# Optimization experiments

Measured on AMD Instinct MI355X. Metric: run time of the kernel, lower is better.

The kernel has to match this reference:

```python
import jax, jax.numpy as jnp
import numpy as np

L_SEG = 20   # number of CFT segments (hard-coded in original forward)
M_CHEB = 8   # Chebyshev quadrature order per segment


def _cft_magnitude(x, modes):
    """|CFT(x)| at integer frequencies [0, modes).

    Faithful to vectorized_batched_cft_decomposed with L=20, M=8, but only
    evaluated at the first `modes` frequencies (identical values; the original
    computes all rfft freqs then slices). Segment loop is folded into a single
    einsum by absorbing the per-segment phase shift into the quadrature weights.
    x: (B, C, N) real. Returns (B, C, modes) float.
    """
    n = x.shape[-1]
    t = jnp.linspace(0.0, 1.0, n)
    freqs = jnp.arange(modes, dtype=x.dtype)  # rfftfreq(n, d=1/n)[:modes]
    seg_len = 1.0 / L_SEG
    starts = jnp.linspace(0.0, 1.0, L_SEG + 1)[:-1]  # (L,)
    k = jnp.arange(M_CHEB, dtype=x.dtype)
    cheb = -jnp.cos((2.0 * k + 1.0) * jnp.pi / (2.0 * M_CHEB))  # (M,) nodes in [-1,1]
    T = jnp.cos(k[:, None] * jnp.arccos(cheb)[None, :])  # (K=M, M) Chebyshev T_k at nodes
    angle = cheb[:, None] * (freqs[None, :] * (2.0 * jnp.pi * seg_len / 2.0))  # (M, F)
    Wr = jnp.einsum('km,mf->kf', T, jnp.cos(angle)) * (seg_len / 2.0)  # (M, F)
    Wi = jnp.einsum('km,mf->kf', T, -jnp.sin(angle)) * (seg_len / 2.0)
    # piecewise-linear interpolation of x at the Chebyshev nodes of every segment
    t_seg = starts[:, None] + seg_len / 2.0 * (cheb + 1.0)[None, :]  # (L, M)
    right = jnp.clip(jnp.searchsorted(t, t_seg), 0, n - 1)
    left = jnp.clip(right - 1, 0, None)
    t_l, t_r = t[left], t[right]
    denom = jnp.where(t_r - t_l == 0.0, 1.0, t_r - t_l)
    w_r = (t_seg - t_l) / denom
    w_l = 1.0 - w_r
    seg = w_l * x[:, :, left] + w_r * x[:, :, right]  # (B, C, L, M)
    # per-segment phase shift exp(-i*2*pi*f*a) folded into combined weights
    phi = 2.0 * jnp.pi * starts[:, None] * freqs[None, :]  # (L, F)
    cs, sn = jnp.cos(phi), jnp.sin(phi)
    Ar = Wr[None] * cs[:, None, :] + Wi[None] * sn[:, None, :]   # (L, M, F)
    Ai = -Wr[None] * sn[:, None, :] + Wi[None] * cs[:, None, :]
    real = jnp.einsum('bclm,lmf->bcf', seg, Ar)
    imag = jnp.einsum('bclm,lmf->bcf', seg, Ai)
    return jnp.sqrt(real * real + imag * imag)


def setup_inputs() -> dict:
    key = jax.random.key(0)
    ks = jax.random.split(key, 4)
    B, Cin, Cout, N, modes = 32, 64, 64, 8192, 32
    scale = 1.0 / (Cin * Cout)
    return {
        'x': jax.random.normal(ks[0], (B, Cin, N), dtype=jnp.float32),
        'w1_real': scale * jax.random.uniform(ks[1], (Cin, Cout, modes), dtype=jnp.float32),
        'w1_imag': scale * jax.random.uniform(ks[2], (Cin, Cout, modes), dtype=jnp.float32),
        'gate_w': jax.random.normal(ks[3], (Cout, Cin), dtype=jnp.float32) / np.sqrt(Cin),
        'ln_gamma': jnp.ones((modes,), dtype=jnp.float32),
        'ln_beta': jnp.zeros((modes,), dtype=jnp.float32),
    }


def reference(x, w1_real, w1_imag, gate_w, ln_gamma, ln_beta):
    n = x.shape[-1]
    n_rfft = n // 2 + 1
    modes = w1_real.shape[-1]
    x_fft = jnp.fft.rfft(x)  # (B, C, n_rfft) complex64
    # CFT magnitude is detached in the original (x_cft.detach())
    mag = jax.lax.stop_gradient(_cft_magnitude(x, modes))  # (B, C, modes)
    # LayerNorm over the modes axis (eps = 1e-5, torch default)
    mu = jnp.mean(mag, axis=-1, keepdims=True)
    var = jnp.mean((mag - mu) ** 2, axis=-1, keepdims=True)
    g_norm = (mag - mu) / jnp.sqrt(var + 1e-5) * ln_gamma + ln_beta
    # 1x1 conv (no bias) over channels, then sigmoid gate
    gate = jax.nn.sigmoid(jnp.einsum('oi,bif->bof', gate_w, g_norm))  # (B, Cout, modes)
    gated = x_fft[:, :, :modes] * gate  # requires Cin == Cout
    w1 = w1_real + 1j * w1_imag  # (Cin, Cout, modes) complex
    out_modes = jnp.einsum('bix,iox->box', gated, w1)
    pad = jnp.zeros(out_modes.shape[:2] + (n_rfft - modes,), dtype=out_modes.dtype)
    out_ft = jnp.concatenate([out_modes, pad], axis=-1)
    return jnp.fft.irfft(out_ft, n=n)
```

## Files before the change

kernel.cpp:

```cpp
#include <hip/hip_runtime.h>
#include <hip/hip_bf16.h>
#include <math.h>

#define NN    8192
#define NH    4096
#define NROWS 2048
#define FF    32
#define LM    160

static constexpr int TRIG   = 0;
static constexpr int W1RT   = 524288;
static constexpr int W1IT   = 655360;
static constexpr int GWT    = 786432;
static constexpr int AR_    = 790528;
static constexpr int AI_    = 795648;
static constexpr int WL_    = 800768;
static constexpr int WR_    = 800928;
static constexpr int IL_    = 801088;
static constexpr int IR_    = 801248;
static constexpr int XR_    = 801408;
static constexpr int XI_    = 866944;
static constexpr int GN_    = 932480;
static constexpr int ARAI   = 998016;
static constexpr int TRIGT_ = 1129088;

#define PI_D 3.14159265358979323846

__device__ __forceinline__ void load_lds16(const float* g, float* l) {
  __builtin_amdgcn_global_load_lds(
      (const __attribute__((address_space(1))) void*)g,
      (__attribute__((address_space(3))) void*)l, 16, 0, 0);
}

__global__ __launch_bounds__(256) void k_trig(float* __restrict__ ws) {
  int idx = blockIdx.x * 256 + threadIdx.x;
  int k4 = idx >> 8, f = (idx >> 2) & 63, e = idx & 3;
  int n = 4 * k4 + e;
  int fr = f & 31;
  int p = (fr * n) & (NN - 1);
  float ang = (float)p * (float)(2.0 * PI_D / (double)NN);
  float s, c;
  sincosf(ang, &s, &c);
  float v = (f < 32) ? c : s;
  ws[TRIG + idx] = v;
  ws[TRIGT_ + f * NH + n] = v;
}

__global__ __launch_bounds__(256) void k_cft_tables(float* __restrict__ ws) {
  int tid = blockIdx.x * 256 + threadIdx.x;
  if (tid >= LM * FF) return;
  int j = tid >> 5, f = tid & 31;
  int l = j >> 3, m = j & 7;
  const double cheb[8] = {
    -0.98078528040323044913, -0.83146961230254523708,
    -0.55557023301960222474, -0.19509032201612826785,
     0.19509032201612826785,  0.55557023301960222474,
     0.83146961230254523708,  0.98078528040323044913 };

  double Wr = 0.0, Wi = 0.0;
  #pragma unroll
  for (int mm = 0; mm < 8; ++mm) {
    double c = cheb[mm];
    double T;
    if (m == 0) T = 1.0;
    else {
      double a = 1.0, b = c;
      for (int q = 1; q < m; ++q) { double t = 2.0 * c * b - a; a = b; b = t; }
      T = b;
    }
    double ang = c * (double)f * (PI_D * 0.05);
    Wr += T * cos(ang);
    Wi += T * (-sin(ang));
  }
  Wr *= 0.025; Wi *= 0.025;
  double phi = 2.0 * PI_D * ((double)l * 0.05) * (double)f;
  double cs = cos(phi), sn = sin(phi);
  ws[AR_ + j * FF + f] = (float)(Wr * cs + Wi * sn);
  ws[AI_ + j * FF + f] = (float)(-Wr * sn + Wi * cs);

  if (f == 0) {
    double v = (double)l * 0.05 + 0.025 * (cheb[m] + 1.0);
    int r = (int)(v * 8191.0);
    while ((double)r / 8191.0 < v) ++r;
    while (r > 0 && (double)(r - 1) / 8191.0 >= v) --r;
    if (r > 8191) r = 8191;
    int le = r - 1; if (le < 0) le = 0;
    double tl = (double)le / 8191.0, tr = (double)r / 8191.0;
    double den = (tr - tl == 0.0) ? 1.0 : (tr - tl);
    double wr = (v - tl) / den;
    ws[WL_ + j] = (float)(1.0 - wr);
    ws[WR_ + j] = (float)wr;
    ((int*)ws)[IL_ + j] = le;
    ((int*)ws)[IR_ + j] = r;
  }
}

__global__ __launch_bounds__(256) void k_transpose(const float* __restrict__ w1r,
                                                   const float* __restrict__ w1i,
                                                   const float* __restrict__ gw,
                                                   float* __restrict__ ws) {
  int idx = blockIdx.x * 256 + threadIdx.x;
  if (idx >= 32 * 64 * 64) return;
  int o = idx & 63, i = (idx >> 6) & 63, f = idx >> 12;
  ws[W1RT + (f * 64 + i) * 64 + o] = w1r[(i * 64 + o) * FF + f];
  ws[W1IT + (f * 64 + i) * 64 + o] = w1i[(i * 64 + o) * FF + f];
  if (idx < 4096) {
    ws[GWT + idx] = gw[(idx & 63) * 64 + (idx >> 6)];
  }
}

__global__ __launch_bounds__(256) void k_fwd_gemm(const float* __restrict__ x,
                                                  const float* __restrict__ ws,
                                                  float* __restrict__ part) {
  __shared__ __align__(16) float uw[4096 + 16 + 4096];
  __shared__ __align__(16) float ts[16 * 256];
  const int rt = blockIdx.x >> 6, jc = blockIdx.x & 63;
  const int t = threadIdx.x;
  const int w = t >> 6, lane = t & 63;
  const int half = lane >> 5, fl = lane & 31;
  const int rblock = rt * 64;
  const int jb = jc * 64;

  const float* __restrict__ tsrc = ws + TRIG + (size_t)jc * 4096;
  #pragma unroll
  for (int p = 0; p < 4; ++p) {
    int q = 256 * p + t;
    load_lds16(tsrc + q * 4, &ts[q * 4]);
  }

  #pragma unroll
  for (int p = 0; p < 4; ++p) {
    int idx = 256 * p + t;
    int row = idx >> 4, c4 = idx & 15;
    const float* __restrict__ xp = x + (size_t)(rblock + row) * NN + jb + c4 * 4;
    float4 a = *(const float4*)xp;
    float4 b = *(const float4*)(xp + NH);
    float4 u = make_float4(a.x + b.x, a.y + b.y, a.z + b.z, a.w + b.w);
    float4 v = make_float4(a.x - b.x, a.y - b.y, a.z - b.z, a.w - b.w);
    *(float4*)(&uw[row * 64 + c4 * 4]) = u;
    *(float4*)(&uw[4112 + row * 64 + c4 * 4]) = v;
  }

  float accC[8], accS[8];
  #pragma unroll
  for (int r = 0; r < 8; ++r) { accC[r] = 0.f; accS[r] = 0.f; }

  __syncthreads();

  const float* __restrict__ xb = &uw[(fl & 1) * 4112 + (w * 16 + half * 8) * 64];
  const float* __restrict__ tb = &ts[fl * 4];

  #pragma unroll
  for (int it = 0; it < 16; ++it) {
    float4 tc = *(const float4*)(tb + it * 256);
    float4 tn = *(const float4*)(tb + it * 256 + 128);
    #pragma unroll
    for (int j = 0; j < 8; ++j) {
      float4 xv = *(const float4*)(xb + j * 64 + it * 4);
      accC[j] = fmaf(xv.w, tc.w, fmaf(xv.z, tc.z,
                fmaf(xv.y, tc.y, fmaf(xv.x, tc.x, accC[j]))));
      accS[j] = fmaf(xv.w, tn.w, fmaf(xv.z, tn.z,
                fmaf(xv.y, tn.y, fmaf(xv.x, tn.x, accS[j]))));
    }
  }

  float* __restrict__ pp = part + ((size_t)jc * NROWS + rblock + w * 16 + half * 8) * 64;
  #pragma unroll
  for (int j = 0; j < 8; ++j) {
    pp[j * 64 + fl]      = accC[j];
    pp[j * 64 + 32 + fl] = accS[j];
  }
}

__global__ __launch_bounds__(256) void k_fred(const float* __restrict__ part,
                                              float* __restrict__ ws) {
  int idx = blockIdx.x * 256 + threadIdx.x;
  int row = idx >> 4, fq = idx & 15;
  const float4* __restrict__ p4 = (const float4*)part;
  float4 s = make_float4(0.f, 0.f, 0.f, 0.f);
  #pragma unroll 16
  for (int kc = 0; kc < 64; ++kc) {
    float4 v = p4[((size_t)kc * NROWS + row) * 16 + fq];
    s.x += v.x; s.y += v.y; s.z += v.z; s.w += v.w;
  }
  if (fq < 8) {
    *(float4*)(ws + XR_ + row * FF + fq * 4) = s;
  } else {
    float4 n = make_float4(-s.x, -s.y, -s.z, -s.w);
    *(float4*)(ws + XI_ + row * FF + (fq - 8) * 4) = n;
  }
}

__global__ __launch_bounds__(256) void k_cft(const float* __restrict__ x,
                                             const float* __restrict__ gamma,
                                             const float* __restrict__ beta,
                                             float* __restrict__ ws) {
  const int sub = threadIdx.x >> 6, li = threadIdx.x & 63;
  const int row = blockIdx.x * 4 + sub;
  const float* __restrict__ xr = x + (size_t)row * NN;
  __shared__ float seg[4][LM];
  #pragma unroll
  for (int g = 0; g < 3; ++g) {
    int j = li + 64 * g;
    if (j < LM) {
      int il = ((const int*)ws)[IL_ + j];
      int ir = ((const int*)ws)[IR_ + j];
      seg[sub][j] = ws[WL_ + j] * xr[il] + ws[WR_ + j] * xr[ir];
    }
  }
  __syncthreads();
  if (li < FF) {
    float re = 0.f, im = 0.f;
    #pragma unroll 8
    for (int j = 0; j < LM; ++j) {
      float sv = seg[sub][j];
      re = fmaf(sv, ws[AR_ + j * FF + li], re);
      im = fmaf(sv, ws[AI_ + j * FF + li], im);
    }
    float mag = sqrtf(re * re + im * im);
    float mu = mag;
    mu += __shfl_xor(mu, 1);  mu += __shfl_xor(mu, 2);  mu += __shfl_xor(mu, 4);
    mu += __shfl_xor(mu, 8);  mu += __shfl_xor(mu, 16);
    mu *= (1.0f / 32.0f);
    float d = mag - mu;
    float vv = d * d;
    vv += __shfl_xor(vv, 1);  vv += __shfl_xor(vv, 2);  vv += __shfl_xor(vv, 4);
    vv += __shfl_xor(vv, 8);  vv += __shfl_xor(vv, 16);
    vv *= (1.0f / 32.0f);
    float g = d / sqrtf(vv + 1e-5f) * gamma[li] + beta[li];
    ws[GN_ + row * FF + li] = g;
  }
}

__global__ __launch_bounds__(64) void k_gate(float* __restrict__ ws) {
  int bidx = blockIdx.x;
  int b = bidx >> 5, f = bidx & 31;
  int o = threadIdx.x;
  __shared__ float gn[64], gr[64], gi[64];
  int rowb = b * 64;
  gn[o] = ws[GN_ + (rowb + o) * FF + f];
  float xre = ws[XR_ + (rowb + o) * FF + f];
  float xim = ws[XI_ + (rowb + o) * FF + f];
  __syncthreads();
  float acc = 0.f;
  #pragma unroll 16
  for (int i = 0; i < 64; ++i)
    acc = fmaf(ws[GWT + i * 64 + o], gn[i], acc);
  float gate = 1.0f / (1.0f + expf(-acc));
  gr[o] = xre * gate;
  gi[o] = xim * gate;
  __syncthreads();
  float Yr = 0.f, Yi = 0.f;
  const float* __restrict__ w1rt = ws + W1RT + f * 4096;
  const float* __restrict__ w1it = ws + W1IT + f * 4096;
  #pragma unroll 8
  for (int i = 0; i < 64; ++i) {
    float a = gr[i], bb2 = gi[i];
    float wr = w1rt[i * 64 + o], wi = w1it[i * 64 + o];
    Yr = fmaf(a, wr, Yr); Yr = fmaf(-bb2, wi, Yr);
    Yi = fmaf(a, wi, Yi); Yi = fmaf(bb2, wr, Yi);
  }
  float* A = ws + ARAI + (size_t)(rowb + o) * 64;
  if (f == 0) {
    A[0]  = Yr * (1.0f / (float)NN);
    A[32] = 0.0f;
  } else {
    A[f]      = Yr * (2.0f / (float)NN);
    A[32 + f] = -Yi * (2.0f / (float)NN);
  }
}

__global__ __launch_bounds__(256) void k_inv(const float* __restrict__ ws,
                                             float* __restrict__ out) {
  __shared__ __align__(16) float As[32 * 64];
  const int blk = blockIdx.x;
  const int bb = blk >> 4, cc = blk & 15;
  const int t = threadIdx.x;
  const int w = t >> 6, lane = t & 63;
  const int rowbase = bb * 32;
  const float* __restrict__ trigt = ws + TRIGT_;
  const int colb = cc * 256 + lane * 4;

  float4 tg0 = *(const float4*)(trigt + (size_t)0 * NH + colb);
  float4 tg1 = *(const float4*)(trigt + (size_t)1 * NH + colb);
  float4 tg2 = *(const float4*)(trigt + (size_t)2 * NH + colb);
  float4 tg3 = *(const float4*)(trigt + (size_t)3 * NH + colb);

  #pragma unroll
  for (int p = 0; p < 2; ++p) {
    int idx = t + 256 * p;
    int r = idx >> 4, q = idx & 15;
    *(float4*)(&As[r * 64 + q * 4]) =
        *(const float4*)(ws + ARAI + (size_t)(rowbase + r) * 64 + q * 4);
  }

  float4 accE[8], accO[8];
  #pragma unroll
  for (int r = 0; r < 8; ++r) {
    accE[r] = make_float4(0.f, 0.f, 0.f, 0.f);
    accO[r] = make_float4(0.f, 0.f, 0.f, 0.f);
  }

  __syncthreads();

#define INV_STEP(F0)                                                            \
  {                                                                             \
    _Pragma("unroll")                                                           \
    for (int r = 0; r < 8; ++r) {                                               \
      float4 av = *(const float4*)(&As[(w * 8 + r) * 64 + (F0)]);               \
      accE[r].x = fmaf(av.x, tg0.x, accE[r].x); accE[r].y = fmaf(av.x, tg0.y, accE[r].y); \
      accE[r].z = fmaf(av.x, tg0.z, accE[r].z); accE[r].w = fmaf(av.x, tg0.w, accE[r].w); \
      accO[r].x = fmaf(av.y, tg1.x, accO[r].x); accO[r].y = fmaf(av.y, tg1.y, accO[r].y); \
      accO[r].z = fmaf(av.y, tg1.z, accO[r].z); accO[r].w = fmaf(av.y, tg1.w, accO[r].w); \
      accE[r].x = fmaf(av.z, tg2.x, accE[r].x); accE[r].y = fmaf(av.z, tg2.y, accE[r].y); \
      accE[r].z = fmaf(av.z, tg2.z, accE[r].z); accE[r].w = fmaf(av.z, tg2.w, accE[r].w); \
      accO[r].x = fmaf(av.w, tg3.x, accO[r].x); accO[r].y = fmaf(av.w, tg3.y, accO[r].y); \
      accO[r].z = fmaf(av.w, tg3.z, accO[r].z); accO[r].w = fmaf(av.w, tg3.w, accO[r].w); \
    }                                                                           \
  }

  for (int fo = 0; fo < 15; ++fo) {
    int f0 = fo * 4;
    float4 n0 = *(const float4*)(trigt + (size_t)(f0 + 4) * NH + colb);
    float4 n1 = *(const float4*)(trigt + (size_t)(f0 + 5) * NH + colb);
    float4 n2 = *(const float4*)(trigt + (size_t)(f0 + 6) * NH + colb);
    float4 n3 = *(const float4*)(trigt + (size_t)(f0 + 7) * NH + colb);
    INV_STEP(f0);
    tg0 = n0; tg1 = n1; tg2 = n2; tg3 = n3;
  }
  INV_STEP(60);
#undef INV_STEP

  #pragma unroll
  for (int r = 0; r < 8; ++r) {
    int row = rowbase + w * 8 + r;
    float4 E = accE[r], O = accO[r];
    float4 s0 = make_float4(E.x + O.x, E.y + O.y, E.z + O.z, E.w + O.w);
    float4 s1 = make_float4(E.x - O.x, E.y - O.y, E.z - O.z, E.w - O.w);
    *(float4*)(out + (size_t)row * NN + colb)      = s0;
    *(float4*)(out + (size_t)row * NN + colb + NH) = s1;
  }
}

extern "C" void kernel_launch(void* const* d_in, const int* in_sizes, int n_in,
                              void* d_out, int out_size, void* d_ws, size_t ws_size,
                              hipStream_t stream) {
  const float* x     = (const float*)d_in[0];
  const float* w1r   = (const float*)d_in[1];
  const float* w1i   = (const float*)d_in[2];
  const float* gw    = (const float*)d_in[3];
  const float* gamma = (const float*)d_in[4];
  const float* beta  = (const float*)d_in[5];
  float* out = (float*)d_out;
  float* ws = (float*)d_ws;
  float* part = (float*)d_out;

  hipLaunchKernelGGL(k_trig,       dim3(1024), dim3(256), 0, stream, ws);
  hipLaunchKernelGGL(k_cft_tables, dim3(20),   dim3(256), 0, stream, ws);
  hipLaunchKernelGGL(k_transpose,  dim3(512),  dim3(256), 0, stream, w1r, w1i, gw, ws);
  hipLaunchKernelGGL(k_fwd_gemm,   dim3(2048), dim3(256), 0, stream, x, ws, part);
  hipLaunchKernelGGL(k_fred,       dim3(128),  dim3(256), 0, stream, part, ws);
  hipLaunchKernelGGL(k_cft,        dim3(512),  dim3(256), 0, stream, x, gamma, beta, ws);
  hipLaunchKernelGGL(k_gate,       dim3(1024), dim3(64),  0, stream, ws);
  hipLaunchKernelGGL(k_inv,        dim3(1024), dim3(256), 0, stream, ws, out);
}
```

Baseline: 179.9 us.

## Merge setup kernels and fold CFT into forward GEMM launch, read trig from global

Merges the three table/transpose kernels into one k_setup launch, and folds the CFT/LayerNorm kernel into the forward DFT GEMM kernel as extra blocks. In the GEMM path, the twiddle table is no longer staged in LDS; each lane now reads it straight from global memory with a one-step register prefetch. This cuts launch count from 8 to 5, lowers LDS use per block, and lets the CFT work overlap the GEMM. The cost is more global or L2 traffic for the twiddles and possible latency stalls in the inner loop.

Result: no change. 178.3 us (-0.9%).

```diff
diff --git a/kernel.cpp b/kernel.cpp
--- a/kernel.cpp
+++ b/kernel.cpp
@@ -26,149 +26,198 @@
 
 #define PI_D 3.14159265358979323846
 
-__device__ __forceinline__ void load_lds16(const float* g, float* l) {
-  __builtin_amdgcn_global_load_lds(
-      (const __attribute__((address_space(1))) void*)g,
-      (__attribute__((address_space(3))) void*)l, 16, 0, 0);
-}
-
-__global__ __launch_bounds__(256) void k_trig(float* __restrict__ ws) {
-  int idx = blockIdx.x * 256 + threadIdx.x;
-  int k4 = idx >> 8, f = (idx >> 2) & 63, e = idx & 3;
-  int n = 4 * k4 + e;
-  int fr = f & 31;
-  int p = (fr * n) & (NN - 1);
-  float ang = (float)p * (float)(2.0 * PI_D / (double)NN);
-  float s, c;
-  sincosf(ang, &s, &c);
-  float v = (f < 32) ? c : s;
-  ws[TRIG + idx] = v;
-  ws[TRIGT_ + f * NH + n] = v;
-}
-
-__global__ __launch_bounds__(256) void k_cft_tables(float* __restrict__ ws) {
-  int tid = blockIdx.x * 256 + threadIdx.x;
-  if (tid >= LM * FF) return;
-  int j = tid >> 5, f = tid & 31;
-  int l = j >> 3, m = j & 7;
-  const double cheb[8] = {
-    -0.98078528040323044913, -0.83146961230254523708,
-    -0.55557023301960222474, -0.19509032201612826785,
-     0.19509032201612826785,  0.55557023301960222474,
-     0.83146961230254523708,  0.98078528040323044913 };
-
-  double Wr = 0.0, Wi = 0.0;
-  #pragma unroll
-  for (int mm = 0; mm < 8; ++mm) {
-    double c = cheb[mm];
-    double T;
-    if (m == 0) T = 1.0;
-    else {
-      double a = 1.0, b = c;
-      for (int q = 1; q < m; ++q) { double t = 2.0 * c * b - a; a = b; b = t; }
-      T = b;
-    }
-    double ang = c * (double)f * (PI_D * 0.05);
-    Wr += T * cos(ang);
-    Wi += T * (-sin(ang));
-  }
-  Wr *= 0.025; Wi *= 0.025;
-  double phi = 2.0 * PI_D * ((double)l * 0.05) * (double)f;
-  double cs = cos(phi), sn = sin(phi);
-  ws[AR_ + j * FF + f] = (float)(Wr * cs + Wi * sn);
-  ws[AI_ + j * FF + f] = (float)(-Wr * sn + Wi * cs);
-
-  if (f == 0) {
-    double v = (double)l * 0.05 + 0.025 * (cheb[m] + 1.0);
-    int r = (int)(v * 8191.0);
-    while ((double)r / 8191.0 < v) ++r;
-    while (r > 0 && (double)(r - 1) / 8191.0 >= v) --r;
-    if (r > 8191) r = 8191;
-    int le = r - 1; if (le < 0) le = 0;
-    double tl = (double)le / 8191.0, tr = (double)r / 8191.0;
-    double den = (tr - tl == 0.0) ? 1.0 : (tr - tl);
-    double wr = (v - tl) / den;
-    ws[WL_ + j] = (float)(1.0 - wr);
-    ws[WR_ + j] = (float)wr;
-    ((int*)ws)[IL_ + j] = le;
-    ((int*)ws)[IR_ + j] = r;
-  }
-}
-
-__global__ __launch_bounds__(256) void k_transpose(const float* __restrict__ w1r,
-                                                   const float* __restrict__ w1i,
-                                                   const float* __restrict__ gw,
-                                                   float* __restrict__ ws) {
-  int idx = blockIdx.x * 256 + threadIdx.x;
-  if (idx >= 32 * 64 * 64) return;
-  int o = idx & 63, i = (idx >> 6) & 63, f = idx >> 12;
-  ws[W1RT + (f * 64 + i) * 64 + o] = w1r[(i * 64 + o) * FF + f];
-  ws[W1IT + (f * 64 + i) * 64 + o] = w1i[(i * 64 + o) * FF + f];
-  if (idx < 4096) {
-    ws[GWT + idx] = gw[(idx & 63) * 64 + (idx >> 6)];
-  }
-}
-
-__global__ __launch_bounds__(256) void k_fwd_gemm(const float* __restrict__ x,
-                                                  const float* __restrict__ ws,
-                                                  float* __restrict__ part) {
-  __shared__ __align__(16) float uw[4096 + 16 + 4096];
-  __shared__ __align__(16) float ts[16 * 256];
-  const int rt = blockIdx.x >> 6, jc = blockIdx.x & 63;
+__global__ __launch_bounds__(256) void k_setup(const float* __restrict__ w1r,
+                                               const float* __restrict__ w1i,
+                                               const float* __restrict__ gw,
+                                               float* __restrict__ ws) {
+  const int bid = blockIdx.x, tid = threadIdx.x;
+
+  if (bid < 1024) {
+    int idx = bid * 256 + tid;
+    int k4 = idx >> 8, f = (idx >> 2) & 63, e = idx & 3;
+    int n = 4 * k4 + e;
+    int fr = f & 31;
+    int p = (fr * n) & (NN - 1);
+    float ang = (float)p * (float)(2.0 * PI_D / (double)NN);
+    float s, c;
+    sincosf(ang, &s, &c);
+    float v = (f < 32) ? c : s;
+    ws[TRIG + idx] = v;
+    ws[TRIGT_ + f * NH + n] = v;
+    return;
+  }
+
+  if (bid < 1044) {
+    int t2 = (bid - 1024) * 256 + tid;
+    if (t2 >= LM * FF) return;
+    int j = t2 >> 5, f = t2 & 31;
+    int l = j >> 3, m = j & 7;
+    const double cheb[8] = {
+      -0.98078528040323044913, -0.83146961230254523708,
+      -0.55557023301960222474, -0.19509032201612826785,
+       0.19509032201612826785,  0.55557023301960222474,
+       0.83146961230254523708,  0.98078528040323044913 };
+
+    double Wr = 0.0, Wi = 0.0;
+    #pragma unroll
+    for (int mm = 0; mm < 8; ++mm) {
+      double c = cheb[mm];
+      double T;
+      if (m == 0) T = 1.0;
+      else {
+        double a = 1.0, b = c;
+        for (int q = 1; q < m; ++q) { double t = 2.0 * c * b - a; a = b; b = t; }
+        T = b;
+      }
+      double ang = c * (double)f * (PI_D * 0.05);
+      Wr += T * cos(ang);
+      Wi += T * (-sin(ang));
+    }
+    Wr *= 0.025; Wi *= 0.025;
+    double phi = 2.0 * PI_D * ((double)l * 0.05) * (double)f;
+    double cs = cos(phi), sn = sin(phi);
+    ws[AR_ + j * FF + f] = (float)(Wr * cs + Wi * sn);
+    ws[AI_ + j * FF + f] = (float)(-Wr * sn + Wi * cs);
+
+    if (f == 0) {
+      double v = (double)l * 0.05 + 0.025 * (cheb[m] + 1.0);
+      int r = (int)(v * 8191.0);
+      while ((double)r / 8191.0 < v) ++r;
+      while (r > 0 && (double)(r - 1) / 8191.0 >= v) --r;
+      if (r > 8191) r = 8191;
+      int le = r - 1; if (le < 0) le = 0;
+      double tl = (double)le / 8191.0, tr = (double)r / 8191.0;
+      double den = (tr - tl == 0.0) ? 1.0 : (tr - tl);
+      double wr = (v - tl) / den;
+      ws[WL_ + j] = (float)(1.0 - wr);
+      ws[WR_ + j] = (float)wr;
+      ((int*)ws)[IL_ + j] = le;
+      ((int*)ws)[IR_ + j] = r;
+    }
+    return;
+  }
+
+  {
+    int idx = (bid - 1044) * 256 + tid;
+    if (idx >= 32 * 64 * 64) return;
+    int o = idx & 63, i = (idx >> 6) & 63, f = idx >> 12;
+    ws[W1RT + (f * 64 + i) * 64 + o] = w1r[(i * 64 + o) * FF + f];
+    ws[W1IT + (f * 64 + i) * 64 + o] = w1i[(i * 64 + o) * FF + f];
+    if (idx < 4096) {
+      ws[GWT + idx] = gw[(idx & 63) * 64 + (idx >> 6)];
+    }
+  }
+}
+
+__global__ __launch_bounds__(256) void k_fwd(const float* __restrict__ x,
+                                             float* __restrict__ ws,
+                                             float* __restrict__ part,
+                                             const float* __restrict__ gamma,
+                                             const float* __restrict__ beta) {
+  __shared__ __align__(16) float smem[4096 + 16 + 4096];
+  const int bid = blockIdx.x;
   const int t = threadIdx.x;
-  const int w = t >> 6, lane = t & 63;
-  const int half = lane >> 5, fl = lane & 31;
-  const int rblock = rt * 64;
-  const int jb = jc * 64;
-
-  const float* __restrict__ tsrc = ws + TRIG + (size_t)jc * 4096;
-  #pragma unroll
-  for (int p = 0; p < 4; ++p) {
-    int q = 256 * p + t;
-    load_lds16(tsrc + q * 4, &ts[q * 4]);
-  }
-
-  #pragma unroll
-  for (int p = 0; p < 4; ++p) {
-    int idx = 256 * p + t;
-    int row = idx >> 4, c4 = idx & 15;
-    const float* __restrict__ xp = x + (size_t)(rblock + row) * NN + jb + c4 * 4;
-    float4 a = *(const float4*)xp;
-    float4 b = *(const float4*)(xp + NH);
-    float4 u = make_float4(a.x + b.x, a.y + b.y, a.z + b.z, a.w + b.w);
-    float4 v = make_float4(a.x - b.x, a.y - b.y, a.z - b.z, a.w - b.w);
-    *(float4*)(&uw[row * 64 + c4 * 4]) = u;
-    *(float4*)(&uw[4112 + row * 64 + c4 * 4]) = v;
-  }
-
-  float accC[8], accS[8];
-  #pragma unroll
-  for (int r = 0; r < 8; ++r) { accC[r] = 0.f; accS[r] = 0.f; }
-
-  __syncthreads();
-
-  const float* __restrict__ xb = &uw[(fl & 1) * 4112 + (w * 16 + half * 8) * 64];
-  const float* __restrict__ tb = &ts[fl * 4];
-
-  #pragma unroll
-  for (int it = 0; it < 16; ++it) {
-    float4 tc = *(const float4*)(tb + it * 256);
-    float4 tn = *(const float4*)(tb + it * 256 + 128);
+
+  if (bid < 2048) {
+    const int rt = bid >> 6, jc = bid & 63;
+    const int w = t >> 6, lane = t & 63;
+    const int half = lane >> 5, fl = lane & 31;
+    const int rblock = rt * 64;
+    const int jb = jc * 64;
+
+    #pragma unroll
+    for (int p = 0; p < 4; ++p) {
+      int idx = 256 * p + t;
+      int row = idx >> 4, c4 = idx & 15;
+      const float* __restrict__ xp = x + (size_t)(rblock + row) * NN + jb + c4 * 4;
+      float4 a = *(const float4*)xp;
+      float4 b = *(const float4*)(xp + NH);
+      float4 u = make_float4(a.x + b.x, a.y + b.y, a.z + b.z, a.w + b.w);
+      float4 v = make_float4(a.x - b.x, a.y - b.y, a.z - b.z, a.w - b.w);
+      *(float4*)(&smem[row * 64 + c4 * 4]) = u;
+      *(float4*)(&smem[4112 + row * 64 + c4 * 4]) = v;
+    }
+
+    float accC[8], accS[8];
+    #pragma unroll
+    for (int r = 0; r < 8; ++r) { accC[r] = 0.f; accS[r] = 0.f; }
+
+    __syncthreads();
+
+    const float* __restrict__ xb = &smem[(fl & 1) * 4112 + (w * 16 + half * 8) * 64];
+    const float4* __restrict__ tg4 = (const float4*)(ws + TRIG);
+    const size_t gb = (size_t)(jc * 16) * 64;
+
+#define FWD_STEP(IT, TC, TS)                                                    \
+    {                                                                           \
+      _Pragma("unroll")                                                         \
+      for (int j = 0; j < 8; ++j) {                                             \
+        float4 xv = *(const float4*)(xb + j * 64 + (IT) * 4);                   \
+        accC[j] = fmaf(xv.w, (TC).w, fmaf(xv.z, (TC).z,                         \
+                  fmaf(xv.y, (TC).y, fmaf(xv.x, (TC).x, accC[j]))));            \
+        accS[j] = fmaf(xv.w, (TS).w, fmaf(xv.z, (TS).z,                         \
+                  fmaf(xv.y, (TS).y, fmaf(xv.x, (TS).x, accS[j]))));            \
+      }                                                                         \
+    }
+
+    float4 tc = tg4[gb + fl];
+    float4 tn = tg4[gb + 32 + fl];
+    #pragma unroll 5
+    for (int it = 0; it < 15; ++it) {
+      float4 tc2 = tg4[gb + (size_t)(it + 1) * 64 + fl];
+      float4 tn2 = tg4[gb + (size_t)(it + 1) * 64 + 32 + fl];
+      FWD_STEP(it, tc, tn);
+      tc = tc2; tn = tn2;
+    }
+    FWD_STEP(15, tc, tn);
+#undef FWD_STEP
+
+    float* __restrict__ pp = part + ((size_t)jc * NROWS + rblock + w * 16 + half * 8) * 64;
     #pragma unroll
     for (int j = 0; j < 8; ++j) {
-      float4 xv = *(const float4*)(xb + j * 64 + it * 4);
-      accC[j] = fmaf(xv.w, tc.w, fmaf(xv.z, tc.z,
-                fmaf(xv.y, tc.y, fmaf(xv.x, tc.x, accC[j]))));
-      accS[j] = fmaf(xv.w, tn.w, fmaf(xv.z, tn.z,
-                fmaf(xv.y, tn.y, fmaf(xv.x, tn.x, accS[j]))));
-    }
-  }
-
-  float* __restrict__ pp = part + ((size_t)jc * NROWS + rblock + w * 16 + half * 8) * 64;
-  #pragma unroll
-  for (int j = 0; j < 8; ++j) {
-    pp[j * 64 + fl]      = accC[j];
-    pp[j * 64 + 32 + fl] = accS[j];
+      pp[j * 64 + fl]      = accC[j];
+      pp[j * 64 + 32 + fl] = accS[j];
+    }
+    return;
+  }
+
+  {
+    const int cb = bid - 2048;
+    const int sub = t >> 6, li = t & 63;
+    const int row = cb * 4 + sub;
+    const float* __restrict__ xr = x + (size_t)row * NN;
+    float (*seg)[LM] = (float (*)[LM])smem;
+    #pragma unroll
+    for (int g = 0; g < 3; ++g) {
+      int j = li + 64 * g;
+      if (j < LM) {
+        int il = ((const int*)ws)[IL_ + j];
+        int ir = ((const int*)ws)[IR_ + j];
+        seg[sub][j] = ws[WL_ + j] * xr[il] + ws[WR_ + j] * xr[ir];
+      }
+    }
+    __syncthreads();
+    if (li < FF) {
+      float re = 0.f, im = 0.f;
+      #pragma unroll 8
+      for (int j = 0; j < LM; ++j) {
+        float sv = seg[sub][j];
+        re = fmaf(sv, ws[AR_ + j * FF + li], re);
+        im = fmaf(sv, ws[AI_ + j * FF + li], im);
+      }
+      float mag = sqrtf(re * re + im * im);
+      float mu = mag;
+      mu += __shfl_xor(mu, 1);  mu += __shfl_xor(mu, 2);  mu += __shfl_xor(mu, 4);
+      mu += __shfl_xor(mu, 8);  mu += __shfl_xor(mu, 16);
+      mu *= (1.0f / 32.0f);
+      float d = mag - mu;
+      float vv = d * d;
+      vv += __shfl_xor(vv, 1);  vv += __shfl_xor(vv, 2);  vv += __shfl_xor(vv, 4);
+      vv += __shfl_xor(vv, 8);  vv += __shfl_xor(vv, 16);
+      vv *= (1.0f / 32.0f);
+      float g = d / sqrtf(vv + 1e-5f) * gamma[li] + beta[li];
+      ws[GN_ + row * FF + li] = g;
+    }
   }
 }
 
@@ -188,47 +237,6 @@
   } else {
     float4 n = make_float4(-s.x, -s.y, -s.z, -s.w);
     *(float4*)(ws + XI_ + row * FF + (fq - 8) * 4) = n;
-  }
-}
-
-__global__ __launch_bounds__(256) void k_cft(const float* __restrict__ x,
-                                             const float* __restrict__ gamma,
-                                             const float* __restrict__ beta,
-                                             float* __restrict__ ws) {
-  const int sub = threadIdx.x >> 6, li = threadIdx.x & 63;
-  const int row = blockIdx.x * 4 + sub;
-  const float* __restrict__ xr = x + (size_t)row * NN;
-  __shared__ float seg[4][LM];
-  #pragma unroll
-  for (int g = 0; g < 3; ++g) {
-    int j = li + 64 * g;
-    if (j < LM) {
-      int il = ((const int*)ws)[IL_ + j];
-      int ir = ((const int*)ws)[IR_ + j];
-      seg[sub][j] = ws[WL_ + j] * xr[il] + ws[WR_ + j] * xr[ir];
-    }
-  }
-  __syncthreads();
-  if (li < FF) {
-    float re = 0.f, im = 0.f;
-    #pragma unroll 8
-    for (int j = 0; j < LM; ++j) {
-      float sv = seg[sub][j];
-      re = fmaf(sv, ws[AR_ + j * FF + li], re);
-      im = fmaf(sv, ws[AI_ + j * FF + li], im);
-    }
-    float mag = sqrtf(re * re + im * im);
-    float mu = mag;
-    mu += __shfl_xor(mu, 1);  mu += __shfl_xor(mu, 2);  mu += __shfl_xor(mu, 4);
-    mu += __shfl_xor(mu, 8);  mu += __shfl_xor(mu, 16);
-    mu *= (1.0f / 32.0f);
-    float d = mag - mu;
-    float vv = d * d;
-    vv += __shfl_xor(vv, 1);  vv += __shfl_xor(vv, 2);  vv += __shfl_xor(vv, 4);
-    vv += __shfl_xor(vv, 8);  vv += __shfl_xor(vv, 16);
-    vv *= (1.0f / 32.0f);
-    float g = d / sqrtf(vv + 1e-5f) * gamma[li] + beta[li];
-    ws[GN_ + row * FF + li] = g;
   }
 }
 
@@ -355,12 +363,9 @@
   float* ws = (float*)d_ws;
   float* part = (float*)d_out;
 
-  hipLaunchKernelGGL(k_trig,       dim3(1024), dim3(256), 0, stream, ws);
-  hipLaunchKernelGGL(k_cft_tables, dim3(20),   dim3(256), 0, stream, ws);
-  hipLaunchKernelGGL(k_transpose,  dim3(512),  dim3(256), 0, stream, w1r, w1i, gw, ws);
-  hipLaunchKernelGGL(k_fwd_gemm,   dim3(2048), dim3(256), 0, stream, x, ws, part);
-  hipLaunchKernelGGL(k_fred,       dim3(128),  dim3(256), 0, stream, part, ws);
-  hipLaunchKernelGGL(k_cft,        dim3(512),  dim3(256), 0, stream, x, gamma, beta, ws);
-  hipLaunchKernelGGL(k_gate,       dim3(1024), dim3(64),  0, stream, ws);
-  hipLaunchKernelGGL(k_inv,        dim3(1024), dim3(256), 0, stream, ws, out);
-}
+  hipLaunchKernelGGL(k_setup, dim3(1556), dim3(256), 0, stream, w1r, w1i, gw, ws);
+  hipLaunchKernelGGL(k_fwd,   dim3(2560), dim3(256), 0, stream, x, ws, part, gamma, beta);
+  hipLaunchKernelGGL(k_fred,  dim3(128),  dim3(256), 0, stream, part, ws);
+  hipLaunchKernelGGL(k_gate,  dim3(1024), dim3(64),  0, stream, ws);
+  hipLaunchKernelGGL(k_inv,   dim3(1024), dim3(256), 0, stream, ws, out);
+}
```
